# Optimization experiments

Measured on AMD Instinct MI355X. Metric: run time of the kernel, lower is better.

## Reference

```python
import jax, jax.numpy as jnp
import numpy as np
from jax import lax

N, D1, D2, H, W = 1, 32, 32, 128, 160


def l1_normalize(k, eps=1e-12):
    # F.normalize(k, p=1, dim=1): divide by max(sum |k|, eps) over channel dim
    denom = jnp.maximum(jnp.sum(jnp.abs(k), axis=1, keepdims=True), eps)
    return k / denom


def _scan_forward(x, k):
    """Recurrent SGA-style scan along axis 2 (forward).
    x: (N, C, S, T) cost slices; k: (N, 5, S, T) normalized guidance.
    out(s) = k0*x(s) + k1*out(s-1) + k2*out_{c-1}(s-1) + k3*out_{c+1}(s-1)
             + k4*max_c out(s-1);  out(0) = x(0) at the boundary.
    """
    xs = jnp.moveaxis(x, 2, 0)   # (S, N, C, T)
    ks = jnp.moveaxis(k, 2, 0)   # (S, N, 5, T)
    init = xs[0]                 # (N, C, T)

    def step(prev, inp):
        xr, kr = inp
        k0, k1, k2, k3, k4 = jnp.split(kr, 5, axis=1)            # each (N,1,T)
        pm1 = jnp.concatenate([jnp.zeros_like(prev[:, :1]), prev[:, :-1]], axis=1)
        pp1 = jnp.concatenate([prev[:, 1:], jnp.zeros_like(prev[:, :1])], axis=1)
        pmx = jnp.max(prev, axis=1, keepdims=True)
        out = k0 * xr + k1 * prev + k2 * pm1 + k3 * pp1 + k4 * pmx
        return out, out

    _, rest = lax.scan(step, init, (xs[1:], ks[1:]))
    out = jnp.concatenate([init[None], rest], axis=0)
    return jnp.moveaxis(out, 0, 2)


def nlf_dir(x, k, axis, reverse):
    """One directional aggregation pass. axis in {2 (H), 3 (W)}."""
    if reverse:
        x = jnp.flip(x, axis); k = jnp.flip(k, axis)
    if axis == 3:
        x = x.swapaxes(2, 3); k = k.swapaxes(2, 3)
    out = _scan_forward(x, k)
    if axis == 3:
        out = out.swapaxes(2, 3)
    if reverse:
        out = jnp.flip(out, axis)
    return out


def nlf_forward(x, g):
    n, d1, d2, h, w = x.shape
    xc = x.reshape(n, d1 * d2, h, w)
    k1, k2, k3, k4 = jnp.split(g, 4, axis=1)
    k1 = l1_normalize(k1); k2 = l1_normalize(k2)
    k3 = l1_normalize(k3); k4 = l1_normalize(k4)
    xc = nlf_dir(xc, k1, axis=2, reverse=False)   # down
    xc = nlf_dir(xc, k2, axis=2, reverse=True)    # up
    xc = nlf_dir(xc, k3, axis=3, reverse=False)   # right
    xc = nlf_dir(xc, k4, axis=3, reverse=True)    # left
    return xc.reshape(n, d1, d2, h, w)


def setup_inputs() -> dict:
    key = jax.random.key(0)
    kx, kg = jax.random.split(key)
    x = jax.random.normal(kx, (N, D1, D2, H, W), dtype=jnp.float32)
    g = jax.random.normal(kg, (N, 20, H, W), dtype=jnp.float32)
    return {"x": x, "g": g}


def reference(x, g):
    return nlf_forward(x, g)
```

## Files before the change

### kernel.cpp

```cpp
#include <hip/hip_runtime.h>

#define Hh 128
#define Ww 160
#define Cc 1024
#define HWp (Hh*Ww)

template<int CTRL>
__device__ __forceinline__ float dppMaxStage(float v) {
    int t = __builtin_amdgcn_update_dpp((int)0xFF800000, __float_as_int(v),
                                        CTRL, 0xF, 0xF, false);
    return fmaxf(v, __int_as_float(t));
}
__device__ __forceinline__ float waveMaxDpp(float v) {
    v = dppMaxStage<0x111>(v);
    v = dppMaxStage<0x112>(v);
    v = dppMaxStage<0x114>(v);
    v = dppMaxStage<0x118>(v);
    v = dppMaxStage<0x142>(v);
    v = dppMaxStage<0x143>(v);
    return __int_as_float(__builtin_amdgcn_readlane(__float_as_int(v), 63));
}
__device__ __forceinline__ float dppRor1(float v) {
    return __int_as_float(__builtin_amdgcn_update_dpp(0, __float_as_int(v),
                                                      0x13C, 0xF, 0xF, false));
}
__device__ __forceinline__ float dppRol1(float v) {
    return __int_as_float(__builtin_amdgcn_update_dpp(0, __float_as_int(v),
                                                      0x134, 0xF, 0xF, false));
}

__global__ __launch_bounds__(256) void norm_g(const float* __restrict__ g,
                                              float* __restrict__ kn)
{
    int p = blockIdx.x * blockDim.x + threadIdx.x;
    if (p >= HWp) return;
    int s = p / Ww, t = p - s * Ww;
    #pragma unroll
    for (int d = 0; d < 4; ++d) {
        float v[5]; float sum = 0.f;
        #pragma unroll
        for (int j = 0; j < 5; ++j) {
            v[j] = g[(size_t)(5 * d + j) * HWp + p];
            sum += fabsf(v[j]);
        }
        float inv = 1.f / fmaxf(sum, 1e-12f);
        size_t off = (d < 2) ? (((size_t)d * HWp + (size_t)t * Hh + s) * 8)
                             : (((size_t)d * HWp + (size_t)p) * 8);
        #pragma unroll
        for (int j = 0; j < 5; ++j) kn[off + j] = v[j] * inv;
        kn[off + 5] = 0.f; kn[off + 6] = 0.f; kn[off + 7] = 0.f;
    }
}

__global__ __launch_bounds__(256) void transpose_in(const float* __restrict__ in,
                                                    float* __restrict__ out)
{
    __shared__ float tile[32][33];
    int p0 = blockIdx.x * 32, c0 = blockIdx.y * 32;
    int tx = threadIdx.x, ty = threadIdx.y;
    #pragma unroll
    for (int i = 0; i < 4; ++i)
        tile[ty + 8 * i][tx] = in[(size_t)(c0 + ty + 8 * i) * HWp + p0 + tx];
    __syncthreads();
    #pragma unroll
    for (int i = 0; i < 4; ++i)
        out[(size_t)(p0 + ty + 8 * i) * Cc + c0 + tx] = tile[tx][ty + 8 * i];
}

__global__ __launch_bounds__(256) void transpose_out(const float* __restrict__ Y,
                                                     float* __restrict__ out)
{
    __shared__ float tile[32][33];
    int c0 = blockIdx.x * 32, p0 = blockIdx.y * 32;
    int tx = threadIdx.x, ty = threadIdx.y;
    #pragma unroll
    for (int i = 0; i < 4; ++i)
        tile[ty + 8 * i][tx] = Y[(size_t)(p0 + ty + 8 * i) * Cc + c0 + tx];
    __syncthreads();
    #pragma unroll
    for (int i = 0; i < 4; ++i)
        out[(size_t)(c0 + ty + 8 * i) * HWp + p0 + tx] = tile[tx][ty + 8 * i];
}

template<int NSTEPS, long STRIDE, long COLSTRIDE, bool FWD>
__global__ __launch_bounds__(64, 1) void scan_pass(float* __restrict__ Y,
                                                   const float* __restrict__ ktab)
{
    __shared__ float ks_raw[Ww * 8 + 16];
    float* ks = ks_raw + 8;
    const int l = threadIdx.x;

    const float* kt = ktab + (size_t)blockIdx.x * (size_t)(NSTEPS * 8);
    #pragma unroll 4
    for (int i = l; i < NSTEPS * 8; i += 64) ks[i] = kt[i];
    __syncthreads();

    constexpr long SSTEP = FWD ? STRIDE : -STRIDE;
    constexpr int  KSTEP = FWD ? 1 : -1;
    long cur = (long)blockIdx.x * COLSTRIDE + (FWD ? 0L : (long)(NSTEPS - 1) * STRIDE);
    int kidx = FWD ? 0 : NSTEPS - 1;
    const int loff = 4 * l;

    float4 prev[4];
    #pragma unroll
    for (int q = 0; q < 4; ++q)
        prev[q] = *reinterpret_cast<const float4*>(&Y[cur + q * 256 + loff]);
    float mx = -3.4e38f;
    #pragma unroll
    for (int q = 0; q < 4; ++q)
        mx = fmaxf(mx, fmaxf(fmaxf(prev[q].x, prev[q].y),
                             fmaxf(prev[q].z, prev[q].w)));
    float pmax = waveMaxDpp(mx);

    float4 xb0[4], xb1[4], xb2[4], xb3[4];
    #pragma unroll
    for (int q = 0; q < 4; ++q)
        xb0[q] = *reinterpret_cast<const float4*>(&Y[cur + 1 * SSTEP + q * 256 + loff]);
    #pragma unroll
    for (int q = 0; q < 4; ++q)
        xb1[q] = *reinterpret_cast<const float4*>(&Y[cur + 2 * SSTEP + q * 256 + loff]);
    #pragma unroll
    for (int q = 0; q < 4; ++q)
        xb2[q] = *reinterpret_cast<const float4*>(&Y[cur + 3 * SSTEP + q * 256 + loff]);
    #pragma unroll
    for (int q = 0; q < 4; ++q)
        xb3[q] = *reinterpret_cast<const float4*>(&Y[cur + 4 * SSTEP + q * 256 + loff]);

    kidx += KSTEP;
    float4 pkv = *reinterpret_cast<const float4*>(&ks[kidx * 8]);
    float  pk4 = ks[kidx * 8 + 4];

    cur += SSTEP;
    int i = 1;

#define STEP(XB)                                                              \
  {                                                                           \
    const float k0 = pkv.x, k1 = pkv.y, k2 = pkv.z, k3 = pkv.w, k4 = pk4;     \
    kidx += KSTEP;                                                            \
    pkv = *reinterpret_cast<const float4*>(&ks[kidx * 8]);                    \
    pk4 = ks[kidx * 8 + 4];                                                   \
    float A[4], B[4];                                                         \
    _Pragma("unroll") for (int q = 0; q < 4; ++q) {                           \
      A[q] = dppRor1(prev[q].w);               \
      B[q] = dppRol1(prev[q].x);               \
    }                                                                         \
    float4 pt[4]; float m = -3.4e38f;                                         \
    _Pragma("unroll") for (int q = 0; q < 4; ++q) {                           \
      float pm0 = (l > 0)  ? A[q] : (q > 0 ? A[q - 1] : 0.f);                 \
      float pp3 = (l < 63) ? B[q] : (q < 3 ? B[q + 1] : 0.f);                 \
      float4 p = prev[q], x = XB[q];                                          \
      pt[q].x = k0 * x.x + k1 * p.x + k2 * pm0 + k3 * p.y;                    \
      pt[q].y = k0 * x.y + k1 * p.y + k2 * p.x + k3 * p.z;                    \
      pt[q].z = k0 * x.z + k1 * p.z + k2 * p.y + k3 * p.w;                    \
      pt[q].w = k0 * x.w + k1 * p.w + k2 * p.z + k3 * pp3;                    \
      m = fmaxf(m, fmaxf(fmaxf(pt[q].x, pt[q].y), fmaxf(pt[q].z, pt[q].w)));  \
    }                                                                         \
    if (i + 4 < NSTEPS) {                                                     \
      _Pragma("unroll") for (int q = 0; q < 4; ++q)                           \
        XB[q] = *reinterpret_cast<const float4*>(                             \
            &Y[cur + 4 * SSTEP + q * 256 + loff]);                            \
    }                                                                         \
    float R = waveMaxDpp(m);                                                  \
    _Pragma("unroll") for (int q = 0; q < 4; ++q) {                           \
      prev[q].x = fmaf(k4, pmax, pt[q].x);                                    \
      prev[q].y = fmaf(k4, pmax, pt[q].y);                                    \
      prev[q].z = fmaf(k4, pmax, pt[q].z);                                    \
      prev[q].w = fmaf(k4, pmax, pt[q].w);                                    \
      *reinterpret_cast<float4*>(&Y[cur + q * 256 + loff]) = prev[q];         \
    }                                                                         \
    pmax = fmaf(k4, pmax, R);                                                 \
    cur += SSTEP; ++i;                                                        \
  }

    while (i + 3 < NSTEPS) { STEP(xb0) STEP(xb1) STEP(xb2) STEP(xb3) }
    if (i < NSTEPS) STEP(xb0)
    if (i < NSTEPS) STEP(xb1)
    if (i < NSTEPS) STEP(xb2)
#undef STEP
}

extern "C" void kernel_launch(void* const* d_in, const int* in_sizes, int n_in,
                              void* d_out, int out_size, void* d_ws, size_t ws_size,
                              hipStream_t stream)
{
    const float* x = (const float*)d_in[0];
    const float* g = (const float*)d_in[1];
    float* out = (float*)d_out;

    const size_t kn_bytes = (size_t)4 * HWp * 8 * sizeof(float);
    const size_t y_bytes  = (size_t)Cc * HWp * sizeof(float);
    if (ws_size < kn_bytes + y_bytes) return;

    float* kn = (float*)d_ws;
    float* Y  = (float*)((char*)d_ws + kn_bytes);

    norm_g<<<(HWp + 255) / 256, 256, 0, stream>>>(g, kn);

    transpose_in<<<dim3(HWp / 32, Cc / 32), dim3(32, 8), 0, stream>>>(x, Y);

    scan_pass<Hh, (long)Ww * Cc, (long)Cc, true ><<<Ww, 64, 0, stream>>>(
        Y, kn + (size_t)0 * HWp * 8);
    scan_pass<Hh, (long)Ww * Cc, (long)Cc, false><<<Ww, 64, 0, stream>>>(
        Y, kn + (size_t)1 * HWp * 8);
    scan_pass<Ww, (long)Cc, (long)Ww * Cc, true ><<<Hh, 64, 0, stream>>>(
        Y, kn + (size_t)2 * HWp * 8);
    scan_pass<Ww, (long)Cc, (long)Ww * Cc, false><<<Hh, 64, 0, stream>>>(
        Y, kn + (size_t)3 * HWp * 8);

    transpose_out<<<dim3(Cc / 32, HWp / 32), dim3(32, 8), 0, stream>>>(Y, out);
}
```

Baseline: 270.7 us.

## Stage 32-step chunks of scan input into LDS before the recurrent loop

The scan kernel now bulk-loads 32 consecutive scan slices (all 1024 channels) into a 128KB shared buffer per chunk, then runs the serial recurrence reading inputs from LDS instead of keeping a 4-deep register prefetch from global memory. The aim is to issue many global loads at once and take global latency off the serial dependency chain. In exchange, load and compute no longer overlap within a chunk, and the large LDS footprint limits residency. It also relies on NSTEPS being divisible by 32 and the LDS size fitting the hardware limit.

```diff
diff --git a/kernel.cpp b/kernel.cpp
--- a/kernel.cpp
+++ b/kernel.cpp
@@ -4,6 +4,8 @@
 #define Ww 160
 #define Cc 1024
 #define HWp (Hh*Ww)
+
+typedef float f4 __attribute__((ext_vector_type(4)));
 
 template<int CTRL>
 __device__ __forceinline__ float dppMaxStage(float v) {
@@ -86,97 +88,118 @@
 __global__ __launch_bounds__(64, 1) void scan_pass(float* __restrict__ Y,
                                                    const float* __restrict__ ktab)
 {
-    __shared__ float ks_raw[Ww * 8 + 16];
+    constexpr int CH = 32;
+    constexpr int NC = NSTEPS / CH;
+    __shared__ float xs[CH * Cc];
+    __shared__ float ks_raw[NSTEPS * 8 + 16];
     float* ks = ks_raw + 8;
     const int l = threadIdx.x;
+    const int loff = 4 * l;
 
     const float* kt = ktab + (size_t)blockIdx.x * (size_t)(NSTEPS * 8);
     #pragma unroll 4
     for (int i = l; i < NSTEPS * 8; i += 64) ks[i] = kt[i];
     __syncthreads();
 
-    constexpr long SSTEP = FWD ? STRIDE : -STRIDE;
-    constexpr int  KSTEP = FWD ? 1 : -1;
-    long cur = (long)blockIdx.x * COLSTRIDE + (FWD ? 0L : (long)(NSTEPS - 1) * STRIDE);
-    int kidx = FWD ? 0 : NSTEPS - 1;
-    const int loff = 4 * l;
-
-    float4 prev[4];
-    #pragma unroll
-    for (int q = 0; q < 4; ++q)
-        prev[q] = *reinterpret_cast<const float4*>(&Y[cur + q * 256 + loff]);
-    float mx = -3.4e38f;
-    #pragma unroll
-    for (int q = 0; q < 4; ++q)
-        mx = fmaxf(mx, fmaxf(fmaxf(prev[q].x, prev[q].y),
-                             fmaxf(prev[q].z, prev[q].w)));
-    float pmax = waveMaxDpp(mx);
-
-    float4 xb0[4], xb1[4], xb2[4], xb3[4];
-    #pragma unroll
-    for (int q = 0; q < 4; ++q)
-        xb0[q] = *reinterpret_cast<const float4*>(&Y[cur + 1 * SSTEP + q * 256 + loff]);
-    #pragma unroll
-    for (int q = 0; q < 4; ++q)
-        xb1[q] = *reinterpret_cast<const float4*>(&Y[cur + 2 * SSTEP + q * 256 + loff]);
-    #pragma unroll
-    for (int q = 0; q < 4; ++q)
-        xb2[q] = *reinterpret_cast<const float4*>(&Y[cur + 3 * SSTEP + q * 256 + loff]);
-    #pragma unroll
-    for (int q = 0; q < 4; ++q)
-        xb3[q] = *reinterpret_cast<const float4*>(&Y[cur + 4 * SSTEP + q * 256 + loff]);
-
-    kidx += KSTEP;
-    float4 pkv = *reinterpret_cast<const float4*>(&ks[kidx * 8]);
-    float  pk4 = ks[kidx * 8 + 4];
-
-    cur += SSTEP;
-    int i = 1;
-
-#define STEP(XB)                                                              \
-  {                                                                           \
-    const float k0 = pkv.x, k1 = pkv.y, k2 = pkv.z, k3 = pkv.w, k4 = pk4;     \
-    kidx += KSTEP;                                                            \
-    pkv = *reinterpret_cast<const float4*>(&ks[kidx * 8]);                    \
-    pk4 = ks[kidx * 8 + 4];                                                   \
-    float A[4], B[4];                                                         \
-    _Pragma("unroll") for (int q = 0; q < 4; ++q) {                           \
-      A[q] = dppRor1(prev[q].w);               \
-      B[q] = dppRol1(prev[q].x);               \
-    }                                                                         \
-    float4 pt[4]; float m = -3.4e38f;                                         \
-    _Pragma("unroll") for (int q = 0; q < 4; ++q) {                           \
-      float pm0 = (l > 0)  ? A[q] : (q > 0 ? A[q - 1] : 0.f);                 \
-      float pp3 = (l < 63) ? B[q] : (q < 3 ? B[q + 1] : 0.f);                 \
-      float4 p = prev[q], x = XB[q];                                          \
-      pt[q].x = k0 * x.x + k1 * p.x + k2 * pm0 + k3 * p.y;                    \
-      pt[q].y = k0 * x.y + k1 * p.y + k2 * p.x + k3 * p.z;                    \
-      pt[q].z = k0 * x.z + k1 * p.z + k2 * p.y + k3 * p.w;                    \
-      pt[q].w = k0 * x.w + k1 * p.w + k2 * p.z + k3 * pp3;                    \
-      m = fmaxf(m, fmaxf(fmaxf(pt[q].x, pt[q].y), fmaxf(pt[q].z, pt[q].w)));  \
-    }                                                                         \
-    if (i + 4 < NSTEPS) {                                                     \
-      _Pragma("unroll") for (int q = 0; q < 4; ++q)                           \
-        XB[q] = *reinterpret_cast<const float4*>(                             \
-            &Y[cur + 4 * SSTEP + q * 256 + loff]);                            \
-    }                                                                         \
-    float R = waveMaxDpp(m);                                                  \
-    _Pragma("unroll") for (int q = 0; q < 4; ++q) {                           \
-      prev[q].x = fmaf(k4, pmax, pt[q].x);                                    \
-      prev[q].y = fmaf(k4, pmax, pt[q].y);                                    \
-      prev[q].z = fmaf(k4, pmax, pt[q].z);                                    \
-      prev[q].w = fmaf(k4, pmax, pt[q].w);                                    \
-      *reinterpret_cast<float4*>(&Y[cur + q * 256 + loff]) = prev[q];         \
-    }                                                                         \
-    pmax = fmaf(k4, pmax, R);                                                 \
-    cur += SSTEP; ++i;                                                        \
-  }
-
-    while (i + 3 < NSTEPS) { STEP(xb0) STEP(xb1) STEP(xb2) STEP(xb3) }
-    if (i < NSTEPS) STEP(xb0)
-    if (i < NSTEPS) STEP(xb1)
-    if (i < NSTEPS) STEP(xb2)
-#undef STEP
+    const long base = (long)blockIdx.x * COLSTRIDE;
+
+    f4 prev[4];
+    float pmax = 0.f;
+
+    for (int c = 0; c < NC; ++c) {
+        #pragma unroll 4
+        for (int j = 0; j < CH; ++j) {
+            const int step = c * CH + j;
+            const long sl = FWD ? (long)step : (long)(NSTEPS - 1 - step);
+            const float* src = Y + base + sl * STRIDE + loff;
+            f4 t0 = *(const f4*)(src + 0);
+            f4 t1 = *(const f4*)(src + 256);
+            f4 t2 = *(const f4*)(src + 512);
+            f4 t3 = *(const f4*)(src + 768);
+            *(f4*)&xs[j * Cc + 0   + loff] = t0;
+            *(f4*)&xs[j * Cc + 256 + loff] = t1;
+            *(f4*)&xs[j * Cc + 512 + loff] = t2;
+            *(f4*)&xs[j * Cc + 768 + loff] = t3;
+        }
+
+        int j0 = 0;
+        if (c == 0) {
+            #pragma unroll
+            for (int q = 0; q < 4; ++q)
+                prev[q] = *(const f4*)&xs[q * 256 + loff];
+            float mx = -3.4e38f;
+            #pragma unroll
+            for (int q = 0; q < 4; ++q)
+                mx = fmaxf(mx, fmaxf(fmaxf(prev[q].x, prev[q].y),
+                                     fmaxf(prev[q].z, prev[q].w)));
+            pmax = waveMaxDpp(mx);
+            j0 = 1;
+        }
+        if (j0 >= CH) continue;
+
+        f4 xq[4];
+        #pragma unroll
+        for (int q = 0; q < 4; ++q)
+            xq[q] = *(const f4*)&xs[j0 * Cc + q * 256 + loff];
+        int step0 = c * CH + j0;
+        int krow = FWD ? step0 : (NSTEPS - 1 - step0);
+        f4 pkv = *(const f4*)&ks[krow * 8];
+        float pk4 = ks[krow * 8 + 4];
+
+        #pragma unroll 4
+        for (int j = j0; j < CH; ++j) {
+            const int step = c * CH + j;
+            const float k0 = pkv.x, k1 = pkv.y, k2 = pkv.z, k3 = pkv.w,
+                        k4 = pk4;
+            const int nk = FWD ? (step + 1) : (NSTEPS - 2 - step);
+            pkv = *(const f4*)&ks[nk * 8];
+            pk4 = ks[nk * 8 + 4];
+
+            f4 xc[4];
+            #pragma unroll
+            for (int q = 0; q < 4; ++q) xc[q] = xq[q];
+            if (j + 1 < CH) {
+                #pragma unroll
+                for (int q = 0; q < 4; ++q)
+                    xq[q] = *(const f4*)&xs[(j + 1) * Cc + q * 256 + loff];
+            }
+
+            float A[4], B[4];
+            #pragma unroll
+            for (int q = 0; q < 4; ++q) {
+                A[q] = dppRor1(prev[q].w);
+                B[q] = dppRol1(prev[q].x);
+            }
+            f4 pt[4]; float m = -3.4e38f;
+            #pragma unroll
+            for (int q = 0; q < 4; ++q) {
+                float pm0 = (l > 0)  ? A[q] : (q > 0 ? A[q - 1] : 0.f);
+                float pp3 = (l < 63) ? B[q] : (q < 3 ? B[q + 1] : 0.f);
+                f4 p = prev[q], x = xc[q];
+                pt[q].x = k0 * x.x + k1 * p.x + k2 * pm0 + k3 * p.y;
+                pt[q].y = k0 * x.y + k1 * p.y + k2 * p.x + k3 * p.z;
+                pt[q].z = k0 * x.z + k1 * p.z + k2 * p.y + k3 * p.w;
+                pt[q].w = k0 * x.w + k1 * p.w + k2 * p.z + k3 * pp3;
+                m = fmaxf(m, fmaxf(fmaxf(pt[q].x, pt[q].y),
+                                   fmaxf(pt[q].z, pt[q].w)));
+            }
+            float R = waveMaxDpp(m);
+            #pragma unroll
+            for (int q = 0; q < 4; ++q) {
+                prev[q].x = fmaf(k4, pmax, pt[q].x);
+                prev[q].y = fmaf(k4, pmax, pt[q].y);
+                prev[q].z = fmaf(k4, pmax, pt[q].z);
+                prev[q].w = fmaf(k4, pmax, pt[q].w);
+            }
+            const long sl = FWD ? (long)step : (long)(NSTEPS - 1 - step);
+            float* dst = Y + base + sl * STRIDE + loff;
+            *(f4*)(dst + 0)   = prev[0];
+            *(f4*)(dst + 256) = prev[1];
+            *(f4*)(dst + 512) = prev[2];
+            *(f4*)(dst + 768) = prev[3];
+            pmax = fmaf(k4, pmax, R);
+        }
+    }
 }
 
 extern "C" void kernel_launch(void* const* d_in, const int* in_sizes, int n_in,
```

Measured after the change: 358.7 us. 32.5% more time.
